# Optimization experiments

Hardware: AMD Instinct MI355X
Metric: run time of the kernel (lower is better)

## Reference

```python
import jax, jax.numpy as jnp
import numpy as np
from jax import lax

H, W = 2048, 2048  # output_size


def setup_inputs() -> dict:
    key = jax.random.key(0)
    # normalized [ymin, xmin, ymax, xmax] in [0,1]; invalid (min>=max) boxes are
    # naturally skipped by the empty-mask logic, same as the torch `continue`.
    boxes = jax.random.uniform(key, (1024, 4), dtype=jnp.float32)
    return {"boxes": boxes}


def reference(boxes):
    ys = jnp.arange(H, dtype=jnp.int32)  # [H]
    xs = jnp.arange(W, dtype=jnp.int32)  # [W]

    def paint(smap, box):
        # pixel coords: truncate toward zero like torch .long(), then clamp
        y1 = jnp.maximum(0, (box[0] * H).astype(jnp.int32))
        x1 = jnp.maximum(0, (box[1] * W).astype(jnp.int32))
        y2 = jnp.minimum(H, (box[2] * H).astype(jnp.int32))
        x2 = jnp.minimum(W, (box[3] * W).astype(jnp.int32))
        cover = ((ys >= y1) & (ys < y2))[:, None] & ((xs >= x1) & (xs < x2))[None, :]  # [H,W]
        # channel values: [1.0, ymin, xmin, ymax, xmax] (normalized box coords)
        vals = jnp.concatenate([jnp.ones((1,), boxes.dtype), box])  # [5]
        # later boxes overwrite earlier ones inside their rectangle (paint order)
        new_map = jnp.where(cover[None, :, :], vals[:, None, None], smap)
        return new_map, None

    smap0 = jnp.zeros((5, H, W), dtype=boxes.dtype)
    smap, _ = lax.scan(paint, smap0, boxes)
    return smap[None]  # (1, 5, H, W)
```

## Files before the change

kernel.cpp:

```cpp
#include <hip/hip_runtime.h>

#define HH 2048
#define WW 2048
#define NB 1024
#define TW 128
#define TH 32

__global__ __launch_bounds__(256, 4) void paint_kernel(const float4* __restrict__ boxes,
                                                       float* __restrict__ out) {
    __shared__ unsigned long long imaskS[4][4];
    __shared__ unsigned long long fmaskS[4][4];
    __shared__ uint2 clist[NB];
    __shared__ short cidxS[NB];

    const int tid  = threadIdx.x;
    const int lane = tid & 63;
    const int wid  = tid >> 6;
    const int tileX = blockIdx.x * TW;
    const int tileY = blockIdx.y * TH;

    int ry1[4], rx1[4], ry2[4], rx2[4];
    bool rint[4];
    #pragma unroll
    for (int c = 0; c < 4; ++c) {
        float4 bx = boxes[c * 256 + tid];
        int y1 = max(0, (int)(bx.x * (float)HH));
        int x1 = max(0, (int)(bx.y * (float)WW));
        int y2 = min(HH, (int)(bx.z * (float)HH));
        int x2 = min(WW, (int)(bx.w * (float)WW));
        ry1[c] = y1; rx1[c] = x1; ry2[c] = y2; rx2[c] = x2;
        bool valid = (y1 < y2) && (x1 < x2);
        bool inter = valid && (y1 < tileY + TH) && (y2 > tileY) &&
                     (x1 < tileX + TW) && (x2 > tileX);
        bool full  = (y1 <= tileY) && (y2 >= tileY + TH) &&
                     (x1 <= tileX) && (x2 >= tileX + TW);
        rint[c] = inter;
        unsigned long long mi = __ballot(inter);
        unsigned long long mf = __ballot(full);
        if (lane == 0) { imaskS[c][wid] = mi; fmaskS[c][wid] = mf; }
    }
    __syncthreads();

    int lastFull = -1;
    #pragma unroll
    for (int c = 3; c >= 0; --c)
        #pragma unroll
        for (int w = 3; w >= 0; --w)
            if (lastFull < 0) {
                unsigned long long m = fmaskS[c][w];
                if (m) lastFull = c * 256 + w * 64 + 63 - __clzll(m);
            }

    int cnt_all = 0;
    int myoff[4];
    #pragma unroll
    for (int c = 0; c < 4; ++c) {
        #pragma unroll
        for (int w = 0; w < 4; ++w) {
            unsigned long long m = imaskS[c][w];
            int d = lastFull - (c * 256 + w * 64);
            if (d >= 63) m = 0;
            else if (d >= 0) m &= (~0ull) << (d + 1);
            if (w == wid)
                myoff[c] = cnt_all + __popcll(m & ((1ull << lane) - 1ull));
            cnt_all += __popcll(m);
        }
    }

    #pragma unroll
    for (int c = 0; c < 4; ++c) {
        int b = c * 256 + tid;
        if (rint[c] && b > lastFull) {
            clist[myoff[c]] = make_uint2(((unsigned)ry1[c] << 16) | (unsigned)rx1[c],
                                         ((unsigned)ry2[c] << 16) | (unsigned)rx2[c]);
            cidxS[myoff[c]] = (short)b;
        }
    }
    __syncthreads();

    const int qx  = tid & 31;
    const int px0 = tileX + qx * 4;
    const int ry  = tid >> 5;
    const int py0 = tileY + ry * 4;

    if (cnt_all == 0) {
        float4 bv = make_float4(0.f, 0.f, 0.f, 0.f);
        float on = 0.f;
        if (lastFull >= 0) { bv = boxes[lastFull]; on = 1.f; }
        float vals[5] = {on, bv.x, bv.y, bv.z, bv.w};
        #pragma unroll
        for (int ch = 0; ch < 5; ++ch) {
            float4 v = make_float4(vals[ch], vals[ch], vals[ch], vals[ch]);
            size_t base = (size_t)ch * (HH * WW);
            #pragma unroll
            for (int s = 0; s < 4; ++s)
                *(float4*)(out + base + (size_t)(py0 + s) * WW + px0) = v;
        }
    } else {
        int fnd[4][4];
        #pragma unroll
        for (int s = 0; s < 4; ++s)
            #pragma unroll
            for (int k = 0; k < 4; ++k) fnd[s][k] = lastFull;
        for (int j = 0; j < cnt_all; ++j) {
            uint2 pc = clist[j];
            int bidx = cidxS[j];
            int by1 = (int)(pc.x >> 16), bx1 = (int)(pc.x & 0xffff);
            int by2 = (int)(pc.y >> 16), bx2 = (int)(pc.y & 0xffff);
            #pragma unroll
            for (int s = 0; s < 4; ++s) {
                int py = py0 + s;
                bool yin = (py >= by1) && (py < by2);
                #pragma unroll
                for (int k = 0; k < 4; ++k) {
                    int px = px0 + k;
                    if (yin && px >= bx1 && px < bx2) fnd[s][k] = bidx;
                }
            }
        }
        #pragma unroll
        for (int s = 0; s < 4; ++s) {
            float4 v[5];
            #pragma unroll
            for (int k = 0; k < 4; ++k) {
                int f = fnd[s][k];
                float4 bv = (f >= 0) ? boxes[f] : make_float4(0.f, 0.f, 0.f, 0.f);
                float on = (f >= 0) ? 1.f : 0.f;
                ((float*)&v[0])[k] = on;
                ((float*)&v[1])[k] = bv.x;
                ((float*)&v[2])[k] = bv.y;
                ((float*)&v[3])[k] = bv.z;
                ((float*)&v[4])[k] = bv.w;
            }
            size_t pb = (size_t)(py0 + s) * WW + px0;
            #pragma unroll
            for (int ch = 0; ch < 5; ++ch)
                *(float4*)(out + (size_t)ch * (HH * WW) + pb) = v[ch];
        }
    }
}

extern "C" void kernel_launch(void* const* d_in, const int* in_sizes, int n_in,
                              void* d_out, int out_size, void* d_ws, size_t ws_size,
                              hipStream_t stream) {
    const float4* boxes = (const float4*)d_in[0];
    float* out = (float*)d_out;
    dim3 grid(WW / TW, HH / TH);
    dim3 block(256);
    paint_kernel<<<grid, block, 0, stream>>>(boxes, out);
}
```

Before: 91.82 us.

## Reshape tiles to 256x16 and gather box values from shared memory

```diff
diff --git a/kernel.cpp b/kernel.cpp
--- a/kernel.cpp
+++ b/kernel.cpp
@@ -3,15 +3,15 @@
 #define HH 2048
 #define WW 2048
 #define NB 1024
-#define TW 128
-#define TH 32
+#define TW 256
+#define TH 16
 
 __global__ __launch_bounds__(256, 4) void paint_kernel(const float4* __restrict__ boxes,
                                                        float* __restrict__ out) {
     __shared__ unsigned long long imaskS[4][4];
     __shared__ unsigned long long fmaskS[4][4];
-    __shared__ uint2 clist[NB];
-    __shared__ short cidxS[NB];
+    __shared__ uint2  clist[NB];
+    __shared__ float4 clistV[NB];
 
     const int tid  = threadIdx.x;
     const int lane = tid & 63;
@@ -19,15 +19,16 @@
     const int tileX = blockIdx.x * TW;
     const int tileY = blockIdx.y * TH;
 
+    float4 bx[4];
     int ry1[4], rx1[4], ry2[4], rx2[4];
     bool rint[4];
     #pragma unroll
     for (int c = 0; c < 4; ++c) {
-        float4 bx = boxes[c * 256 + tid];
-        int y1 = max(0, (int)(bx.x * (float)HH));
-        int x1 = max(0, (int)(bx.y * (float)WW));
-        int y2 = min(HH, (int)(bx.z * (float)HH));
-        int x2 = min(WW, (int)(bx.w * (float)WW));
+        bx[c] = boxes[c * 256 + tid];
+        int y1 = max(0, (int)(bx[c].x * (float)HH));
+        int x1 = max(0, (int)(bx[c].y * (float)WW));
+        int y2 = min(HH, (int)(bx[c].z * (float)HH));
+        int x2 = min(WW, (int)(bx[c].w * (float)WW));
         ry1[c] = y1; rx1[c] = x1; ry2[c] = y2; rx2[c] = x2;
         bool valid = (y1 < y2) && (x1 < x2);
         bool inter = valid && (y1 < tileY + TH) && (y2 > tileY) &&
@@ -71,23 +72,22 @@
     for (int c = 0; c < 4; ++c) {
         int b = c * 256 + tid;
         if (rint[c] && b > lastFull) {
-            clist[myoff[c]] = make_uint2(((unsigned)ry1[c] << 16) | (unsigned)rx1[c],
-                                         ((unsigned)ry2[c] << 16) | (unsigned)rx2[c]);
-            cidxS[myoff[c]] = (short)b;
+            clist[myoff[c]]  = make_uint2(((unsigned)ry1[c] << 16) | (unsigned)rx1[c],
+                                          ((unsigned)ry2[c] << 16) | (unsigned)rx2[c]);
+            clistV[myoff[c]] = bx[c];
         }
     }
     __syncthreads();
 
-    const int qx  = tid & 31;
-    const int px0 = tileX + qx * 4;
-    const int ry  = tid >> 5;
-    const int py0 = tileY + ry * 4;
+    float4 bvLast = make_float4(0.f, 0.f, 0.f, 0.f);
+    float  onLast = 0.f;
+    if (lastFull >= 0) { bvLast = boxes[lastFull]; onLast = 1.f; }
+
+    const int px0 = tileX + lane * 4;
+    const int py0 = tileY + wid * 4;
 
     if (cnt_all == 0) {
-        float4 bv = make_float4(0.f, 0.f, 0.f, 0.f);
-        float on = 0.f;
-        if (lastFull >= 0) { bv = boxes[lastFull]; on = 1.f; }
-        float vals[5] = {on, bv.x, bv.y, bv.z, bv.w};
+        float vals[5] = {onLast, bvLast.x, bvLast.y, bvLast.z, bvLast.w};
         #pragma unroll
         for (int ch = 0; ch < 5; ++ch) {
             float4 v = make_float4(vals[ch], vals[ch], vals[ch], vals[ch]);
@@ -101,10 +101,9 @@
         #pragma unroll
         for (int s = 0; s < 4; ++s)
             #pragma unroll
-            for (int k = 0; k < 4; ++k) fnd[s][k] = lastFull;
+            for (int k = 0; k < 4; ++k) fnd[s][k] = -1;
         for (int j = 0; j < cnt_all; ++j) {
             uint2 pc = clist[j];
-            int bidx = cidxS[j];
             int by1 = (int)(pc.x >> 16), bx1 = (int)(pc.x & 0xffff);
             int by2 = (int)(pc.y >> 16), bx2 = (int)(pc.y & 0xffff);
             #pragma unroll
@@ -114,7 +113,7 @@
                 #pragma unroll
                 for (int k = 0; k < 4; ++k) {
                     int px = px0 + k;
-                    if (yin && px >= bx1 && px < bx2) fnd[s][k] = bidx;
+                    if (yin && px >= bx1 && px < bx2) fnd[s][k] = j;
                 }
             }
         }
@@ -124,8 +123,8 @@
             #pragma unroll
             for (int k = 0; k < 4; ++k) {
                 int f = fnd[s][k];
-                float4 bv = (f >= 0) ? boxes[f] : make_float4(0.f, 0.f, 0.f, 0.f);
-                float on = (f >= 0) ? 1.f : 0.f;
+                float4 bv = (f >= 0) ? clistV[f] : bvLast;
+                float on  = (f >= 0) ? 1.f : onLast;
                 ((float*)&v[0])[k] = on;
                 ((float*)&v[1])[k] = bv.x;
                 ((float*)&v[2])[k] = bv.y;
```

Measured after the change: 94.96 us. 3.4% more time.
